# Kernel optimization log

Hardware: AMD Instinct MI355X
Metric: run time of the kernel (lower is better)

Reference implementation:

```python
import jax, jax.numpy as jnp
import numpy as np

N_QUBITS = 4
N_SEL_LAYERS = 2  # StronglyEntanglingLayers depth; ranges default = (l % (n-1)) + 1


def _apply_1q_batched(state, gate, wire):
    # state: (B, 2,2,2,2) complex; gate: (B, 2, 2) complex, per-row gate
    s = jnp.moveaxis(state, wire + 1, -1)
    s = jnp.einsum('b...i,bji->b...j', s, gate)
    return jnp.moveaxis(s, -1, wire + 1)


def _apply_1q(state, gate, wire):
    # state: (B, 2,2,2,2); gate: (2, 2) shared across batch
    s = jnp.moveaxis(state, wire + 1, -1)
    s = s @ gate.T
    return jnp.moveaxis(s, -1, wire + 1)


def _cnot(state, c, t):
    # flip target axis where control bit == 1
    s = jnp.moveaxis(state, (c + 1, t + 1), (1, 2))
    s = jnp.concatenate([s[:, :1], jnp.flip(s[:, 1:], axis=2)], axis=1)
    return jnp.moveaxis(s, (1, 2), (c + 1, t + 1))


def _rot_gate(w):
    # PennyLane Rot(phi, theta, omega) = RZ(omega) RY(theta) RZ(phi)
    phi, theta, omega = w[0], w[1], w[2]
    c = jnp.cos(theta * 0.5)
    s = jnp.sin(theta * 0.5)
    g00 = jnp.exp(-0.5j * (phi + omega)) * c
    g01 = -jnp.exp(0.5j * (phi - omega)) * s
    g10 = jnp.exp(-0.5j * (phi - omega)) * s
    g11 = jnp.exp(0.5j * (phi + omega)) * c
    return jnp.stack([jnp.stack([g00, g01]), jnp.stack([g10, g11])])  # (2,2) complex64


def _qnode(inputs, weights):
    # inputs: (B, 4) angles; weights: (2, 4, 3). Returns <Z_0> per row, (B,)
    B = inputs.shape[0]
    state = jnp.zeros((B, 16), jnp.complex64).at[:, 0].set(1.0)
    state = state.reshape((B,) + (2,) * N_QUBITS)
    # AngleEmbedding: default rotation='X' -> RX(inputs[w]) on wire w
    half = 0.5 * inputs
    for w in range(N_QUBITS):
        c = jnp.cos(half[:, w]).astype(jnp.complex64)
        s = (-1j) * jnp.sin(half[:, w]).astype(jnp.complex64)
        gate = jnp.stack([jnp.stack([c, s], -1), jnp.stack([s, c], -1)], -2)  # (B,2,2)
        state = _apply_1q_batched(state, gate, w)
    # StronglyEntanglingLayers: Rot on each wire, then ring of CNOTs with range r
    for l in range(N_SEL_LAYERS):
        for w in range(N_QUBITS):
            state = _apply_1q(state, _rot_gate(weights[l, w]), w)
        r = (l % (N_QUBITS - 1)) + 1
        for w in range(N_QUBITS):
            state = _cnot(state, w, (w + r) % N_QUBITS)
    sr = state.reshape(B, 2, 8)
    p = jnp.sum(sr.real ** 2 + sr.imag ** 2, axis=-1)  # (B, 2) marginal of wire 0
    return p[:, 0] - p[:, 1]


def _quad(x, weights):
    # x: (B, N, F) with F % 4 == 0 -> flatten to 4-wide circuit rows (literal view(-1,4))
    B = x.shape[0]
    flat = x.reshape(-1, N_QUBITS)
    out = _qnode(flat, weights)
    return out.reshape(B, -1, 1)


def _regroup(x, h):
    # 'b (h w) c -> b c h w' then 'b c (h h2)(w w2) -> b (h w) (h2 w2 c)', h2=w2=2
    B, N, C = x.shape
    w = N // h
    x = x.reshape(B, h // 2, 2, w // 2, 2, C)
    x = x.transpose(0, 1, 3, 2, 4, 5)  # (B, h/2, w/2, h2, w2, C)
    return x.reshape(B, (h // 2) * (w // 2), 4 * C)


def setup_inputs() -> dict:
    key = jax.random.key(0)
    ks = jax.random.split(key, 8)
    B = 8192
    two_pi = float(2.0 * np.pi)
    x = jax.random.normal(ks[0], (B, 1, 32, 32), jnp.float32)
    We = jax.random.normal(ks[1], (16, 4), jnp.float32) * 0.25   # nn.Linear(16, 4)
    be = jnp.zeros((4,), jnp.float32)
    w1 = jax.random.uniform(ks[2], (2, 4, 3), jnp.float32, 0.0, two_pi)
    w2 = jax.random.uniform(ks[3], (2, 4, 3), jnp.float32, 0.0, two_pi)
    w3 = jax.random.uniform(ks[4], (2, 4, 3), jnp.float32, 0.0, two_pi)
    Wh = jax.random.normal(ks[5], (1, 10), jnp.float32)          # nn.Linear(1, 10)
    bh = jnp.zeros((10,), jnp.float32)
    return {"x": x, "We": We, "be": be, "w1": w1, "w2": w2, "w3": w3, "Wh": Wh, "bh": bh}


def reference(x, We, be, w1, w2, w3, Wh, bh):
    B = x.shape[0]
    # 'b c (h p1) (w p2) -> b (h w) (p1 p2 c)', p1=p2=4, c=1, img 32 -> 8x8 patches
    p = x.reshape(B, 1, 8, 4, 8, 4).transpose(0, 2, 4, 3, 5, 1).reshape(B, 64, 16)
    h = jnp.tanh(p @ We + be)  # (B, 64, 4)
    curr_h = 8
    for w in (w1, w2, w3):
        h = _regroup(h, curr_h)
        h = _quad(h, w)
        curr_h //= 2
    # head Linear(1, 10) applied on trailing singleton feature dim: (B, 4, 1) -> (B, 4, 10)
    return h @ Wh + bh
```

## Files before the change

kernel.cpp:

```cpp
#include <hip/hip_runtime.h>
#include <math.h>

#define NELEM 16

__device__ __forceinline__ void make_gate(float phi, float th, float om, float* g) {
  float ct, st, cp, sp, cm, sm;
  __sincosf(0.5f * th, &st, &ct);
  __sincosf(0.5f * (phi + om), &sp, &cp);
  __sincosf(0.5f * (phi - om), &sm, &cm);
  g[0] =  cp * ct; g[1] = -sp * ct;
  g[2] = -cm * st; g[3] = -sm * st;
  g[4] =  cm * st; g[5] = -sm * st;
  g[6] =  cp * ct; g[7] =  sp * ct;
}

__device__ __forceinline__ float fast_tanh(float x) {
  float e = __expf(2.0f * x);
  return __builtin_fmaf(-2.0f, __builtin_amdgcn_rcpf(e + 1.0f), 1.0f);
}

__device__ __forceinline__ float circuit18(float a0, float a1, float a2, float a3,
                                           const float* __restrict__ K) {
  float s0, c0, s1, c1, s2, c2, s3, c3;
  __sincosf(a0, &s0, &c0);
  __sincosf(a1, &s1, &c1);
  __sincosf(a2, &s2, &c2);
  __sincosf(a3, &s3, &c3);
  float t0  = K[0] * c0 + K[1] * s0;
  float t1  = K[2] * c1 + K[3] * s1;
  float t2  = K[4] * c2 + K[5] * s2;
  float k2r = K[6] + K[7] * c2 + K[8] * s2;
  float k2i = K[9] + K[10] * c2 + K[11] * s2;
  float k3r = K[12] + K[13] * c3 + K[14] * s3;
  float tt = t0 * t1;
  return K[15] * (tt * t2) + k3r * (K[16] * k2r + K[17] * (tt * k2i));
}

__global__ __launch_bounds__(256, 2) void fused_ttn(
    const float* __restrict__ x, const float* __restrict__ We,
    const float* __restrict__ be, const float* __restrict__ w1,
    const float* __restrict__ w2, const float* __restrict__ w3,
    const float* __restrict__ Wh, const float* __restrict__ bh,
    float* __restrict__ out, int B) {
  __shared__ __align__(16) float sC[3][20];
  __shared__ __align__(16) float sWe[64];
  __shared__ float sbe[4];
  __shared__ float sWh[10];
  __shared__ float sbh[10];
  __shared__ float qbuf[NELEM * 65];
  __shared__ float q2buf[NELEM * 17];
  __shared__ float e3buf[NELEM * 4];

  const int t = threadIdx.x;
  const int wv = t >> 6, lane = t & 63;
  const int ph = lane >> 3, pw = lane & 7;

  float4 xv[16];
  const float4* xb = (const float4*)x;
#pragma unroll
  for (int it = 0; it < 4; ++it) {
    size_t gb = (size_t)blockIdx.x * NELEM + (it * 4 + wv);
    if (gb >= (size_t)B) gb = 0;
#pragma unroll
    for (int p1 = 0; p1 < 4; ++p1)
      xv[it * 4 + p1] = xb[gb * 256 + (ph * 4 + p1) * 8 + pw];
  }

  if (t < 12) {
    int s = t >> 2, w = t & 3;
    const float* W = (s == 0) ? w1 : (s == 1) ? w2 : w3;
    float g[8];
    make_gate(W[w * 3], W[w * 3 + 1], W[w * 3 + 2], g);
    float* K = &sC[s][0];
    float Qt = g[0] * g[0] + g[1] * g[1] - g[4] * g[4] - g[5] * g[5];
    float Rt = (g[0] * g[3] - g[1] * g[2]) - (g[4] * g[7] - g[5] * g[6]);
    if (w < 2) {
      K[w * 2] = Qt; K[w * 2 + 1] = Rt;
    } else if (w == 2) {
      K[4] = Qt; K[5] = Rt;
      float u  = g[0] * g[4] + g[1] * g[5], v  = g[2] * g[6] + g[3] * g[7];
      float p  = g[0] * g[5] - g[1] * g[4], q  = g[2] * g[7] - g[3] * g[6];
      float r1 = g[2] * g[4] + g[3] * g[5], m1 = g[2] * g[5] - g[3] * g[4];
      float r2 = g[0] * g[6] + g[1] * g[7], m2 = g[0] * g[7] - g[1] * g[6];
      K[6] = 0.5f * (u + v);  K[7]  = 0.5f * (u - v);  K[8]  = 0.5f * (m2 - m1);
      K[9] = 0.5f * (p + q);  K[10] = 0.5f * (p - q);  K[11] = 0.5f * (r1 - r2);
    } else {
      float u  = g[0] * g[4] + g[1] * g[5], v  = g[2] * g[6] + g[3] * g[7];
      float m1 = g[2] * g[5] - g[3] * g[4], m2 = g[0] * g[7] - g[1] * g[6];
      K[12] = 0.5f * (u + v); K[13] = 0.5f * (u - v); K[14] = 0.5f * (m2 - m1);
    }
  } else if (t < 15) {
    int s = t - 12;
    const float* W = (s == 0) ? w1 : (s == 1) ? w2 : w3;
    float g[8];
    make_gate(W[18], W[19], W[20], g);
    float A    = g[0] * g[0] + g[1] * g[1] - g[4] * g[4] - g[5] * g[5];
    float M01r = g[0] * g[2] + g[1] * g[3] - (g[4] * g[6] + g[5] * g[7]);
    float M01i = (g[0] * g[3] - g[1] * g[2]) - (g[4] * g[7] - g[5] * g[6]);
    sC[s][15] = A; sC[s][16] = 4.0f * M01r; sC[s][17] = -4.0f * M01i;
  }
  if (t < 64) sWe[t] = We[t];
  if (t < 4)  sbe[t] = be[t];
  if (t < 10) { sWh[t] = Wh[t]; sbh[t] = bh[t]; }
  __syncthreads();

  const int grp = (ph >> 1) * 4 + (pw >> 1);
  const int sub = (ph & 1) * 2 + (pw & 1);
  float be0 = sbe[0], be1 = sbe[1], be2 = sbe[2], be3 = sbe[3];
#pragma unroll
  for (int it = 0; it < 4; ++it) {
    float a0 = be0, a1 = be1, a2 = be2, a3 = be3;
#pragma unroll
    for (int p1 = 0; p1 < 4; ++p1) {
      float4 v = xv[it * 4 + p1];
      float vv[4] = {v.x, v.y, v.z, v.w};
#pragma unroll
      for (int p2 = 0; p2 < 4; ++p2) {
        int f = p1 * 4 + p2;
        a0 = __builtin_fmaf(vv[p2], sWe[f * 4 + 0], a0);
        a1 = __builtin_fmaf(vv[p2], sWe[f * 4 + 1], a1);
        a2 = __builtin_fmaf(vv[p2], sWe[f * 4 + 2], a2);
        a3 = __builtin_fmaf(vv[p2], sWe[f * 4 + 3], a3);
      }
    }
    float e1 = circuit18(fast_tanh(a0), fast_tanh(a1), fast_tanh(a2),
                         fast_tanh(a3), &sC[0][0]);
    qbuf[(it * 4 + wv) * 65 + grp * 4 + sub] = e1;
  }
  __syncthreads();

  {
    int e2 = t >> 4, c = t & 15;
    int base = e2 * 65 + (c >> 3) * 32 + (c & 7) * 2;
    float r = circuit18(qbuf[base], qbuf[base + 1], qbuf[base + 16],
                        qbuf[base + 17], &sC[1][0]);
    q2buf[e2 * 17 + c] = r;
  }
  __syncthreads();

  if (t < 64) {
    int e3 = t >> 2, c = t & 3;
    int base = e3 * 17 + c * 2;
    float r = circuit18(q2buf[base], q2buf[base + 1], q2buf[base + 8],
                        q2buf[base + 9], &sC[2][0]);
    e3buf[e3 * 4 + c] = r;
  }
  __syncthreads();

  size_t ob = (size_t)blockIdx.x * (NELEM * 40);
#pragma unroll
  for (int rpt = 0; rpt < 3; ++rpt) {
    int o = t + rpt * 256;
    if (o < NELEM * 40) {
      int eo = o / 40;
      int j  = o - eo * 40;
      int g3 = j / 10;
      int k  = j - g3 * 10;
      int b  = blockIdx.x * NELEM + eo;
      if (b < B) out[ob + o] = e3buf[eo * 4 + g3] * sWh[k] + sbh[k];
    }
  }
}

extern "C" void kernel_launch(void* const* d_in, const int* in_sizes, int n_in,
                              void* d_out, int out_size, void* d_ws, size_t ws_size,
                              hipStream_t stream) {
  (void)n_in; (void)out_size; (void)d_ws; (void)ws_size;
  const float* x  = (const float*)d_in[0];
  const float* We = (const float*)d_in[1];
  const float* be = (const float*)d_in[2];
  const float* w1 = (const float*)d_in[3];
  const float* w2 = (const float*)d_in[4];
  const float* w3 = (const float*)d_in[5];
  const float* Wh = (const float*)d_in[6];
  const float* bh = (const float*)d_in[7];
  float* out = (float*)d_out;

  int B = in_sizes[0] / 1024;
  int blocks = (B + NELEM - 1) / NELEM;
  hipLaunchKernelGGL(fused_ttn, dim3(blocks), dim3(256), 0, stream,
                     x, We, be, w1, w2, w3, Wh, bh, out, B);
}
```

Measured before the change: 12.62 us.

## Process four batch elements per block instead of sixteen

Shrinks each block from sixteen to four batch elements, so each wave handles one element instead of looping over four. The grid grows fourfold (2048 blocks instead of 512), launch bounds rise to four blocks per SIMD, and the per-thread register array drops from 16 to 4 float4 loads. The aim is more blocks and waves in flight to hide memory latency across the 256 CUs. In exchange, the per-block gate-coefficient setup, weight staging to shared memory and barriers are now repeated for four times as many blocks, and later stages leave more threads idle.

```diff
diff --git a/kernel.cpp b/kernel.cpp
--- a/kernel.cpp
+++ b/kernel.cpp
@@ -1,7 +1,7 @@
 #include <hip/hip_runtime.h>
 #include <math.h>
 
-#define NELEM 16
+#define NELEM 4
 
 __device__ __forceinline__ void make_gate(float phi, float th, float om, float* g) {
   float ct, st, cp, sp, cm, sm;
@@ -36,7 +36,7 @@
   return K[15] * (tt * t2) + k3r * (K[16] * k2r + K[17] * (tt * k2i));
 }
 
-__global__ __launch_bounds__(256, 2) void fused_ttn(
+__global__ __launch_bounds__(256, 4) void fused_ttn(
     const float* __restrict__ x, const float* __restrict__ We,
     const float* __restrict__ be, const float* __restrict__ w1,
     const float* __restrict__ w2, const float* __restrict__ w3,
@@ -55,16 +55,13 @@
   const int wv = t >> 6, lane = t & 63;
   const int ph = lane >> 3, pw = lane & 7;
 
-  float4 xv[16];
+  float4 xv[4];
   const float4* xb = (const float4*)x;
+  size_t gb = (size_t)blockIdx.x * NELEM + wv;
+  if (gb >= (size_t)B) gb = 0;
 #pragma unroll
-  for (int it = 0; it < 4; ++it) {
-    size_t gb = (size_t)blockIdx.x * NELEM + (it * 4 + wv);
-    if (gb >= (size_t)B) gb = 0;
-#pragma unroll
-    for (int p1 = 0; p1 < 4; ++p1)
-      xv[it * 4 + p1] = xb[gb * 256 + (ph * 4 + p1) * 8 + pw];
-  }
+  for (int p1 = 0; p1 < 4; ++p1)
+    xv[p1] = xb[gb * 256 + (ph * 4 + p1) * 8 + pw];
 
   if (t < 12) {
     int s = t >> 2, w = t & 3;
@@ -106,30 +103,26 @@
 
   const int grp = (ph >> 1) * 4 + (pw >> 1);
   const int sub = (ph & 1) * 2 + (pw & 1);
-  float be0 = sbe[0], be1 = sbe[1], be2 = sbe[2], be3 = sbe[3];
+  float a0 = sbe[0], a1 = sbe[1], a2 = sbe[2], a3 = sbe[3];
 #pragma unroll
-  for (int it = 0; it < 4; ++it) {
-    float a0 = be0, a1 = be1, a2 = be2, a3 = be3;
+  for (int p1 = 0; p1 < 4; ++p1) {
+    float4 v = xv[p1];
+    float vv[4] = {v.x, v.y, v.z, v.w};
 #pragma unroll
-    for (int p1 = 0; p1 < 4; ++p1) {
-      float4 v = xv[it * 4 + p1];
-      float vv[4] = {v.x, v.y, v.z, v.w};
-#pragma unroll
-      for (int p2 = 0; p2 < 4; ++p2) {
-        int f = p1 * 4 + p2;
-        a0 = __builtin_fmaf(vv[p2], sWe[f * 4 + 0], a0);
-        a1 = __builtin_fmaf(vv[p2], sWe[f * 4 + 1], a1);
-        a2 = __builtin_fmaf(vv[p2], sWe[f * 4 + 2], a2);
-        a3 = __builtin_fmaf(vv[p2], sWe[f * 4 + 3], a3);
-      }
+    for (int p2 = 0; p2 < 4; ++p2) {
+      int f = p1 * 4 + p2;
+      a0 = __builtin_fmaf(vv[p2], sWe[f * 4 + 0], a0);
+      a1 = __builtin_fmaf(vv[p2], sWe[f * 4 + 1], a1);
+      a2 = __builtin_fmaf(vv[p2], sWe[f * 4 + 2], a2);
+      a3 = __builtin_fmaf(vv[p2], sWe[f * 4 + 3], a3);
     }
-    float e1 = circuit18(fast_tanh(a0), fast_tanh(a1), fast_tanh(a2),
-                         fast_tanh(a3), &sC[0][0]);
-    qbuf[(it * 4 + wv) * 65 + grp * 4 + sub] = e1;
   }
+  float e1 = circuit18(fast_tanh(a0), fast_tanh(a1), fast_tanh(a2),
+                       fast_tanh(a3), &sC[0][0]);
+  qbuf[wv * 65 + grp * 4 + sub] = e1;
   __syncthreads();
 
-  {
+  if (t < NELEM * 16) {
     int e2 = t >> 4, c = t & 15;
     int base = e2 * 65 + (c >> 3) * 32 + (c & 7) * 2;
     float r = circuit18(qbuf[base], qbuf[base + 1], qbuf[base + 16],
@@ -138,7 +131,7 @@
   }
   __syncthreads();
 
-  if (t < 64) {
+  if (t < NELEM * 4) {
     int e3 = t >> 2, c = t & 3;
     int base = e3 * 17 + c * 2;
     float r = circuit18(q2buf[base], q2buf[base + 1], q2buf[base + 8],
@@ -147,18 +140,14 @@
   }
   __syncthreads();
 
-  size_t ob = (size_t)blockIdx.x * (NELEM * 40);
-#pragma unroll
-  for (int rpt = 0; rpt < 3; ++rpt) {
-    int o = t + rpt * 256;
-    if (o < NELEM * 40) {
-      int eo = o / 40;
-      int j  = o - eo * 40;
-      int g3 = j / 10;
-      int k  = j - g3 * 10;
-      int b  = blockIdx.x * NELEM + eo;
-      if (b < B) out[ob + o] = e3buf[eo * 4 + g3] * sWh[k] + sbh[k];
-    }
+  if (t < NELEM * 40) {
+    int eo = t / 40;
+    int j  = t - eo * 40;
+    int g3 = j / 10;
+    int k  = j - g3 * 10;
+    int b  = blockIdx.x * NELEM + eo;
+    if (b < B) out[(size_t)blockIdx.x * (NELEM * 40) + t] =
+        e3buf[eo * 4 + g3] * sWh[k] + sbh[k];
   }
 }
 
```

After: 11.66 us. 7.6% less time.
